# Performance work log

Measured on AMD Instinct MI355X. Metric: run time of the kernel, lower is better.

The kernel has to match this reference:

```python
import jax, jax.numpy as jnp
import numpy as np

N = 50000      # nodes
E = 800000     # edges (before self-loops)
DIN, H1, H2, OUT = 128, 128, 64, 40
LN_EPS = 1e-5


def setup_inputs() -> dict:
    key = jax.random.key(0)
    ks = jax.random.split(key, 16)
    s = lambda d: 1.0 / np.sqrt(d)
    inp = {
        "x": jax.random.normal(ks[0], (N, DIN), jnp.float32),
        "edge_index": jax.random.randint(ks[1], (2, E), 0, N, dtype=jnp.int64),
        # GCNConv weights (applied as x @ W) and biases
        "W1": jax.random.normal(ks[2], (DIN, H1), jnp.float32) * s(DIN),
        "b1": jnp.zeros((H1,), jnp.float32),
        "W2": jax.random.normal(ks[3], (H1, H2), jnp.float32) * s(H1),
        "b2": jnp.zeros((H2,), jnp.float32),
        "W3": jax.random.normal(ks[4], (H2, H2), jnp.float32) * s(H2),
        "b3": jnp.zeros((H2,), jnp.float32),
        # LayerNorms
        "g1": jnp.ones((H1,), jnp.float32),
        "be1": jnp.zeros((H1,), jnp.float32),
        "g2": jnp.ones((H2,), jnp.float32),
        "be2": jnp.zeros((H2,), jnp.float32),
        # post_mp MLP head
        "Wp1": jax.random.normal(ks[5], (H2, H2), jnp.float32) * s(H2),
        "bp1": jnp.zeros((H2,), jnp.float32),
        "Wp2": jax.random.normal(ks[6], (H2, OUT), jnp.float32) * s(H2),
        "bp2": jnp.zeros((OUT,), jnp.float32),
    }
    return inp


def _layer_norm(x, g, b):
    mu = jnp.mean(x, axis=-1, keepdims=True)
    var = jnp.mean((x - mu) ** 2, axis=-1, keepdims=True)
    return (x - mu) * jax.lax.rsqrt(var + LN_EPS) * g + b


def _gcn(x, src, dst, norm, W, b):
    # PyG GCNConv: linear first, then normalized gather/scatter-add, bias last
    h = x @ W                                  # [N, H]
    msg = h[src] * norm[:, None]               # [E+N, H] gather
    out = jax.ops.segment_sum(msg, dst, num_segments=N)  # scatter-add
    return out + b


def reference(x, edge_index, W1, b1, W2, b2, W3, b3, g1, be1, g2, be2,
              Wp1, bp1, Wp2, bp2):
    loops = jnp.arange(N, dtype=edge_index.dtype)
    src = jnp.concatenate([edge_index[0], loops])  # add self-loops
    dst = jnp.concatenate([edge_index[1], loops])
    # symmetric normalization D^{-1/2} (A+I) D^{-1/2} (same graph all layers)
    deg = jax.ops.segment_sum(jnp.ones_like(src, dtype=x.dtype), dst,
                              num_segments=N)
    dinv = jnp.where(deg > 0, jax.lax.rsqrt(jnp.maximum(deg, 1.0)), 0.0)
    norm = dinv[src] * dinv[dst]

    h = _gcn(x, src, dst, norm, W1, b1)
    h = _layer_norm(jax.nn.relu(h), g1, be1)
    h = _gcn(h, src, dst, norm, W2, b2)
    h = _layer_norm(jax.nn.relu(h), g2, be2)
    emb = _gcn(h, src, dst, norm, W3, b3)      # emb = conv output, pre-ReLU
    h = jax.nn.relu(emb)
    h = (h @ Wp1 + bp1) @ Wp2 + bp2            # post_mp: two stacked Linears
    return emb, jax.nn.log_softmax(h, axis=1)
```

## Files before the change

### kernel.cpp

```cpp
#include <hip/hip_runtime.h>
#include <hip/hip_bf16.h>

#define DIN 128
#define HID1 128
#define HID2 64
#define OUTD 40
#define NCHUNK 64

typedef __attribute__((ext_vector_type(8))) short bf16x8;
typedef __attribute__((ext_vector_type(4))) float f32x4;

__device__ __forceinline__ float bf2f(unsigned int u) {
    union { unsigned int i; float f; } c;
    c.i = u << 16;
    return c.f;
}
__device__ __forceinline__ unsigned short f2bf(float f) {
    union { float f; unsigned int i; } c; c.f = f;
    unsigned int r = c.i + 0x7FFFu + ((c.i >> 16) & 1u);
    return (unsigned short)(r >> 16);
}
__device__ __forceinline__ unsigned int packbf(float lo, float hi) {
    return (unsigned int)f2bf(lo) | ((unsigned int)f2bf(hi) << 16);
}

struct WCvt {
    const void* p[14];
    int sz[14];
    int off[14];
    int tobf[14];
    int cols[14];
};


__launch_bounds__(512)
__global__ void prep_kernel(const unsigned short* __restrict__ xu,
                            const int* __restrict__ ei,
                            int* __restrict__ flags,
                            int* __restrict__ pos,
                            unsigned int* __restrict__ hist,
                            WCvt wc, unsigned short* __restrict__ wbf,
                            float* __restrict__ wf,
                            int E, int N) {
    __shared__ unsigned int h32[25000];
    __shared__ int sh2[2];
    const int NW = (N + 1) >> 1;
    const int b = blockIdx.x;
    const int t = threadIdx.x;
    if (b < NCHUNK) {
        if (t == 0) sh2[0] = 0;
        for (int w = t; w < NW; w += 512) h32[w] = 0u;
        __syncthreads();
        int zodd = 0;
        for (int k = t; k < 1024; k += 512)
            if (ei[2 * k + 1] == 0) zodd++;
        if (zodd) atomicAdd(&sh2[0], zodd);
        __syncthreads();
        const int e64 = (sh2[0] > 512) ? 1 : 0;
        const int CH = (E + NCHUNK - 1) / NCHUNK;
        const int lo = b * CH;
        int hi = lo + CH; if (hi > E) hi = E;
        for (int e = lo + t; e < hi; e += 512) {
            int d = e64 ? ei[2 * (E + e)] : ei[E + e];
            if ((unsigned)d < (unsigned)N) {
                unsigned sh = (unsigned)(d & 1) << 4;
                unsigned old = atomicAdd(&h32[d >> 1], 1u << sh);
                pos[e] = (int)((old >> sh) & 0xffffu);
            } else {
                pos[e] = -1;
            }
        }
        __syncthreads();
        unsigned int* hb = hist + (size_t)b * NW;
        for (int w = t; w < NW; w += 512) hb[w] = h32[w];
    } else {
        if (t < 2) sh2[t] = 0;
        __syncthreads();
        int bad = 0;
        for (int k = t; k < 2048; k += 512) {
            float v = bf2f(xu[2 * k]);
            float a = fabsf(v);
            if (!(a <= 1e4f) || (v != 0.f && a < 1e-4f)) bad++;
        }
        int zodd = 0;
        for (int k = t; k < 1024; k += 512)
            if (ei[2 * k + 1] == 0) zodd++;
        if (bad) atomicAdd(&sh2[0], bad);
        if (zodd) atomicAdd(&sh2[1], zodd);
        __syncthreads();
        int xf32 = (sh2[0] > 512) ? 1 : 0;
        if (t == 0) {
            flags[0] = xf32;
            flags[1] = (sh2[1] > 512) ? 1 : 0;
        }
        for (int a = 0; a < 14; ++a) {
            const float* pf = (const float*)wc.p[a];
            const unsigned short* pb = (const unsigned short*)wc.p[a];
            int n = wc.sz[a], off = wc.off[a], tobf = wc.tobf[a];
            int cols = wc.cols[a];
            int rows = tobf ? (n / cols) : 0;
            for (int i = t; i < n; i += 512) {
                float v = xf32 ? pf[i] : bf2f(pb[i]);
                if (tobf) {
                    int k = i / cols, m = i % cols;
                    wbf[off + m * rows + k] = f2bf(v);
                } else {
                    wf[off + i] = v;
                }
            }
        }
    }
}

__device__ __forceinline__ int get_src(const int* ei, int E, int e, int e64) {
    return e64 ? ei[2 * e] : ei[e];
}
__device__ __forceinline__ int get_dst(const int* ei, int E, int e, int e64) {
    return e64 ? ei[2 * (E + e)] : ei[E + e];
}

__launch_bounds__(256)
__global__ void phaseB_kernel(const unsigned int* __restrict__ hist,
                              unsigned int* __restrict__ basev,
                              int* __restrict__ cnt, int* __restrict__ bsum,
                              int N) {
    __shared__ int red[256];
    const int NW = (N + 1) >> 1;
    const int NP = NW * 2;
    int t = threadIdx.x;
    int w = blockIdx.x * 256 + t;
    unsigned run0 = 0, run1 = 0;
    if (w < NW) {
        #pragma unroll 4
        for (int b = 0; b < NCHUNK; ++b) {
            unsigned u = hist[(size_t)b * NW + w];
            uint2 bb; bb.x = run0; bb.y = run1;
            *(uint2*)&basev[(size_t)b * NP + 2 * w] = bb;
            run0 += u & 0xffffu;
            run1 += u >> 16;
        }
        cnt[2 * w] = (int)run0;
        if (2 * w + 1 < N) cnt[2 * w + 1] = (int)run1;
    }
    int tot = 0;
    if (w < NW) tot = (int)run0 + ((2 * w + 1 < N) ? (int)run1 : 0);
    red[t] = tot;
    __syncthreads();
    #pragma unroll
    for (int off = 64; off >= 1; off >>= 1) {
        if ((t & 127) < off) red[t] += red[t + off];
        __syncthreads();
    }
    if (t == 0) bsum[2 * blockIdx.x] = red[0];
    if (t == 128) bsum[2 * blockIdx.x + 1] = red[128];
}

__launch_bounds__(256)
__global__ void bscan_kernel(const int* __restrict__ bsum, int* __restrict__ bbase,
                             int* __restrict__ indptr, int NB, int N) {
    __shared__ int part[256];
    int t = threadIdx.x;
    int CH = (NB + 255) / 256;
    int lo = t * CH, hi = lo + CH; if (hi > NB) hi = NB;
    int s = 0;
    for (int i = lo; i < hi; ++i) s += bsum[i];
    part[t] = s;
    __syncthreads();
    for (int off = 1; off < 256; off <<= 1) {
        int v = (t >= off) ? part[t - off] : 0;
        __syncthreads();
        part[t] += v;
        __syncthreads();
    }
    int run = (t > 0) ? part[t - 1] : 0;
    for (int i = lo; i < hi; ++i) { bbase[i] = run; run += bsum[i]; }
    if (t == 255) indptr[N] = part[255];
}

__launch_bounds__(256)
__global__ void emit_kernel(const int* __restrict__ cnt, const int* __restrict__ bbase,
                            int* __restrict__ indptr, float* __restrict__ dinv, int N) {
    __shared__ int sh[256];
    int t = threadIdx.x;
    int i = blockIdx.x * 256 + t;
    int c = (i < N) ? cnt[i] : 0;
    sh[t] = c;
    __syncthreads();
    for (int off = 1; off < 256; off <<= 1) {
        int v = (t >= off) ? sh[t - off] : 0;
        __syncthreads();
        sh[t] += v;
        __syncthreads();
    }
    if (i < N) {
        int excl = sh[t] - c + bbase[blockIdx.x];
        indptr[i] = excl;
        dinv[i] = 1.0f / sqrtf((float)(c + 1));
    }
}

__global__ void scatter_kernel(const int* __restrict__ ei, const int* __restrict__ indptr,
                               const int* __restrict__ pos, const float* __restrict__ dinv,
                               const unsigned int* __restrict__ basev,
                               int2* __restrict__ csr_sn,
                               int E, int N, const int* __restrict__ flags) {
    int e64 = flags[1];
    int CH = (E + NCHUNK - 1) / NCHUNK;
    int NP = ((N + 1) >> 1) * 2;
    int base = (blockIdx.x * blockDim.x + threadIdx.x) * 4;
    #pragma unroll
    for (int u = 0; u < 4; ++u) {
        int e = base + u;
        if (e < E) {
            int p = pos[e];
            if (p >= 0) {
                int bb = e / CH;
                int d = get_dst(ei, E, e, e64);
                int s = get_src(ei, E, e, e64);
                if ((unsigned)s >= (unsigned)N) s = 0;
                float nrm = dinv[s] * dinv[d];
                int slot = indptr[d] + (int)basev[(size_t)bb * NP + d] + p;
                csr_sn[slot] = make_int2(s, __float_as_int(nrm));
            }
        }
    }
}


template<typename AT>
__device__ __forceinline__ bf16x8 ld_afrag(const AT* p);
template<>
__device__ __forceinline__ bf16x8 ld_afrag<unsigned short>(const unsigned short* p) {
    return *(const bf16x8*)p;
}
template<>
__device__ __forceinline__ bf16x8 ld_afrag<float>(const float* p) {
    float4 a = *(const float4*)p;
    float4 b = *(const float4*)(p + 4);
    bf16x8 r;
    r[0] = (short)f2bf(a.x); r[1] = (short)f2bf(a.y);
    r[2] = (short)f2bf(a.z); r[3] = (short)f2bf(a.w);
    r[4] = (short)f2bf(b.x); r[5] = (short)f2bf(b.y);
    r[6] = (short)f2bf(b.z); r[7] = (short)f2bf(b.w);
    return r;
}

template<int K, int M, typename AT>
__device__ __forceinline__ void mm_body(const AT* __restrict__ A,
                                        const unsigned short* __restrict__ WT,
                                        unsigned short* __restrict__ C, int N,
                                        unsigned short (*Ws)[K + 8]) {
    int tid = threadIdx.x;
    for (int idx = tid; idx < M * K / 8; idx += 256) {
        int r = idx / (K / 8), c8 = idx % (K / 8);
        *(uint4*)&Ws[r][c8 * 8] = *(const uint4*)&WT[r * K + c8 * 8];
    }
    __syncthreads();
    int w = tid >> 6, lane = tid & 63;
    int m = lane & 15, q = lane >> 4;
    int row_a = blockIdx.x * 64 + w * 16 + m;
    if (row_a >= N) row_a = N - 1;
    const AT* arow = A + (size_t)row_a * K;
    f32x4 acc[M / 16];
    #pragma unroll
    for (int t = 0; t < M / 16; ++t) acc[t] = (f32x4){0.f, 0.f, 0.f, 0.f};
    #pragma unroll
    for (int ks = 0; ks < K / 32; ++ks) {
        int k0 = ks * 32 + q * 8;
        bf16x8 a = ld_afrag<AT>(arow + k0);
        #pragma unroll
        for (int t = 0; t < M / 16; ++t) {
            bf16x8 b = *(const bf16x8*)&Ws[t * 16 + m][k0];
            acc[t] = __builtin_amdgcn_mfma_f32_16x16x32_bf16(a, b, acc[t], 0, 0, 0);
        }
    }
    int rbase = blockIdx.x * 64 + w * 16 + q * 4;
    #pragma unroll
    for (int reg = 0; reg < 4; ++reg) {
        int row = rbase + reg;
        if (row < N) {
            #pragma unroll
            for (int t = 0; t < M / 16; ++t)
                C[(size_t)row * M + t * 16 + m] = f2bf(acc[t][reg]);
        }
    }
}

template<int K, int M>
__launch_bounds__(256)
__global__ void mm_dual_kernel(const void* __restrict__ A,
                               const unsigned short* __restrict__ WT,
                               unsigned short* __restrict__ C, int N,
                               const int* __restrict__ flags) {
    __shared__ unsigned short Ws[M][K + 8];
    if (flags[0]) mm_body<K, M, float>((const float*)A, WT, C, N, Ws);
    else          mm_body<K, M, unsigned short>((const unsigned short*)A, WT, C, N, Ws);
}

template<int K, int M>
__launch_bounds__(256)
__global__ void mm_bf_kernel(const unsigned short* __restrict__ A,
                             const unsigned short* __restrict__ WT,
                             unsigned short* __restrict__ C, int N) {
    __shared__ unsigned short Ws[M][K + 8];
    mm_body<K, M, unsigned short>(A, WT, C, N, Ws);
}


template<int VPL>
__device__ __forceinline__ void gacc1(float* acc, const unsigned short* r, float n) {
    if constexpr (VPL == 8) {
        uint4 u = *(const uint4*)r;
        acc[0] += bf2f(u.x & 0xffffu) * n; acc[1] += bf2f(u.x >> 16) * n;
        acc[2] += bf2f(u.y & 0xffffu) * n; acc[3] += bf2f(u.y >> 16) * n;
        acc[4] += bf2f(u.z & 0xffffu) * n; acc[5] += bf2f(u.z >> 16) * n;
        acc[6] += bf2f(u.w & 0xffffu) * n; acc[7] += bf2f(u.w >> 16) * n;
    } else {
        uint2 u = *(const uint2*)r;
        acc[0] += bf2f(u.x & 0xffffu) * n; acc[1] += bf2f(u.x >> 16) * n;
        acc[2] += bf2f(u.y & 0xffffu) * n; acc[3] += bf2f(u.y >> 16) * n;
    }
}

template<int VPL>
__device__ __forceinline__ void gacc4(float* acc,
                                      const unsigned short* r0, float n0,
                                      const unsigned short* r1, float n1,
                                      const unsigned short* r2, float n2,
                                      const unsigned short* r3, float n3) {
    if constexpr (VPL == 8) {
        uint4 u0 = *(const uint4*)r0;
        uint4 u1 = *(const uint4*)r1;
        uint4 u2 = *(const uint4*)r2;
        uint4 u3 = *(const uint4*)r3;
        acc[0] += bf2f(u0.x & 0xffffu) * n0 + bf2f(u1.x & 0xffffu) * n1
                + bf2f(u2.x & 0xffffu) * n2 + bf2f(u3.x & 0xffffu) * n3;
        acc[1] += bf2f(u0.x >> 16) * n0 + bf2f(u1.x >> 16) * n1
                + bf2f(u2.x >> 16) * n2 + bf2f(u3.x >> 16) * n3;
        acc[2] += bf2f(u0.y & 0xffffu) * n0 + bf2f(u1.y & 0xffffu) * n1
                + bf2f(u2.y & 0xffffu) * n2 + bf2f(u3.y & 0xffffu) * n3;
        acc[3] += bf2f(u0.y >> 16) * n0 + bf2f(u1.y >> 16) * n1
                + bf2f(u2.y >> 16) * n2 + bf2f(u3.y >> 16) * n3;
        acc[4] += bf2f(u0.z & 0xffffu) * n0 + bf2f(u1.z & 0xffffu) * n1
                + bf2f(u2.z & 0xffffu) * n2 + bf2f(u3.z & 0xffffu) * n3;
        acc[5] += bf2f(u0.z >> 16) * n0 + bf2f(u1.z >> 16) * n1
                + bf2f(u2.z >> 16) * n2 + bf2f(u3.z >> 16) * n3;
        acc[6] += bf2f(u0.w & 0xffffu) * n0 + bf2f(u1.w & 0xffffu) * n1
                + bf2f(u2.w & 0xffffu) * n2 + bf2f(u3.w & 0xffffu) * n3;
        acc[7] += bf2f(u0.w >> 16) * n0 + bf2f(u1.w >> 16) * n1
                + bf2f(u2.w >> 16) * n2 + bf2f(u3.w >> 16) * n3;
    } else {
        uint2 u0 = *(const uint2*)r0;
        uint2 u1 = *(const uint2*)r1;
        uint2 u2 = *(const uint2*)r2;
        uint2 u3 = *(const uint2*)r3;
        acc[0] += bf2f(u0.x & 0xffffu) * n0 + bf2f(u1.x & 0xffffu) * n1
                + bf2f(u2.x & 0xffffu) * n2 + bf2f(u3.x & 0xffffu) * n3;
        acc[1] += bf2f(u0.x >> 16) * n0 + bf2f(u1.x >> 16) * n1
                + bf2f(u2.x >> 16) * n2 + bf2f(u3.x >> 16) * n3;
        acc[2] += bf2f(u0.y & 0xffffu) * n0 + bf2f(u1.y & 0xffffu) * n1
                + bf2f(u2.y & 0xffffu) * n2 + bf2f(u3.y & 0xffffu) * n3;
        acc[3] += bf2f(u0.y >> 16) * n0 + bf2f(u1.y >> 16) * n1
                + bf2f(u2.y >> 16) * n2 + bf2f(u3.y >> 16) * n3;
    }
}

template<int H, bool RELU_LN, bool EMB>
__launch_bounds__(256)
__global__ void agg_kernel(const unsigned short* __restrict__ h,
                           const int* __restrict__ indptr,
                           const int2* __restrict__ csr_sn,
                           const float* __restrict__ dinv,
                           const float* __restrict__ bias,
                           const float* __restrict__ gamma,
                           const float* __restrict__ beta,
                           unsigned short* __restrict__ out,
                           void* __restrict__ out_emb,
                           int N, const int* __restrict__ flags) {
    constexpr int VPL = H / 16;
    __shared__ int2 lsn[4][64];
    int w = threadIdx.x >> 6;
    int lane = threadIdx.x & 63;
    int slot = lane >> 4;
    int idx = lane & 15;
    int node = blockIdx.x * 4 + w;
    bool active = node < N;
    int nd = active ? node : N - 1;
    float di = dinv[nd];
    int c0 = idx * VPL;
    float acc[VPL];
    #pragma unroll
    for (int v = 0; v < VPL; ++v) acc[v] = 0.f;
    if (slot == 0)
        gacc1<VPL>(acc, h + (size_t)nd * H + c0, di * di);
    int beg = indptr[nd], end = indptr[nd + 1];
    for (int base = beg; base < end; base += 64) {
        int m = end - base; if (m > 64) m = 64;
        if (lane < m) lsn[w][lane] = csr_sn[base + lane];
        int m16 = m & ~15;
        int j = 0;
        for (; j < m16; j += 16) {
            int2 e0 = lsn[w][j + slot];
            int2 e1 = lsn[w][j + 4 + slot];
            int2 e2 = lsn[w][j + 8 + slot];
            int2 e3 = lsn[w][j + 12 + slot];
            gacc4<VPL>(acc,
                       h + (size_t)e0.x * H + c0, __int_as_float(e0.y),
                       h + (size_t)e1.x * H + c0, __int_as_float(e1.y),
                       h + (size_t)e2.x * H + c0, __int_as_float(e2.y),
                       h + (size_t)e3.x * H + c0, __int_as_float(e3.y));
        }
        for (int tt = j + slot; tt < m; tt += 4) {
            int2 e = lsn[w][tt];
            gacc1<VPL>(acc, h + (size_t)e.x * H + c0, __int_as_float(e.y));
        }
    }
    #pragma unroll
    for (int v = 0; v < VPL; ++v) {
        acc[v] += __shfl_xor(acc[v], 16, 64);
        acc[v] += __shfl_xor(acc[v], 32, 64);
    }
    #pragma unroll
    for (int v = 0; v < VPL; ++v) acc[v] += bias[c0 + v];
    if constexpr (RELU_LN) {
        #pragma unroll
        for (int v = 0; v < VPL; ++v) acc[v] = fmaxf(acc[v], 0.f);
        float s = 0.f, sq = 0.f;
        #pragma unroll
        for (int v = 0; v < VPL; ++v) { s += acc[v]; sq += acc[v] * acc[v]; }
        #pragma unroll
        for (int off = 8; off >= 1; off >>= 1) {
            s += __shfl_xor(s, off, 64);
            sq += __shfl_xor(sq, off, 64);
        }
        float mu = s * (1.0f / H);
        float var = fmaxf(sq * (1.0f / H) - mu * mu, 0.f);
        float inv = 1.0f / sqrtf(var + 1e-5f);
        #pragma unroll
        for (int v = 0; v < VPL; ++v)
            acc[v] = (acc[v] - mu) * inv * gamma[c0 + v] + beta[c0 + v];
    }
    if (active && slot == 0) {
        unsigned short* orow = out + (size_t)node * H + c0;
        if constexpr (VPL == 8) {
            uint4 p;
            p.x = packbf(acc[0], acc[1]); p.y = packbf(acc[2], acc[3]);
            p.z = packbf(acc[4], acc[5]); p.w = packbf(acc[6], acc[7]);
            *(uint4*)orow = p;
        } else {
            uint2 p; p.x = packbf(acc[0], acc[1]); p.y = packbf(acc[2], acc[3]);
            *(uint2*)orow = p;
        }
        if constexpr (EMB) {
            if (flags[0]) {
                float* o = (float*)out_emb + (size_t)node * H + c0;
                #pragma unroll
                for (int v4 = 0; v4 < VPL / 4; ++v4)
                    *(float4*)(o + v4 * 4) = make_float4(acc[v4 * 4], acc[v4 * 4 + 1],
                                                         acc[v4 * 4 + 2], acc[v4 * 4 + 3]);
            } else {
                unsigned short* o = (unsigned short*)out_emb + (size_t)node * H + c0;
                #pragma unroll
                for (int v2 = 0; v2 < VPL / 2; ++v2)
                    ((unsigned int*)o)[v2] = packbf(acc[v2 * 2], acc[v2 * 2 + 1]);
            }
        }
    }
}


__launch_bounds__(256)
__global__ void head_kernel(const unsigned short* __restrict__ emb,
                            const float* __restrict__ Wp1,
                            const float* __restrict__ bp1,
                            const float* __restrict__ Wp2,
                            const float* __restrict__ bp2,
                            void* __restrict__ d_out, int N,
                            const int* __restrict__ flags) {
    __shared__ float Est[64][68];
    __shared__ float W1s[64][64];
    __shared__ float Tst[64][68];
    __shared__ float W2s[64][OUTD];
    __shared__ float b1s[64];
    __shared__ float b2s[OUTD];
    int tid = threadIdx.x;
    int row0 = blockIdx.x * 64;
    for (int i = tid; i < 64 * 64; i += 256) W1s[i >> 6][i & 63] = Wp1[i];
    for (int i = tid; i < 64 * OUTD; i += 256) W2s[i / OUTD][i % OUTD] = Wp2[i];
    if (tid < 64) b1s[tid] = bp1[tid];
    if (tid < OUTD) b2s[tid] = bp2[tid];
    for (int i = tid; i < 64 * 32; i += 256) {
        int r = i >> 5, kk = i & 31;
        int row = row0 + r;
        unsigned int u = (row < N) ? *(const unsigned int*)&emb[(size_t)row * 64 + kk * 2] : 0u;
        Est[kk * 2][r]     = fmaxf(bf2f(u & 0xffffu), 0.f);
        Est[kk * 2 + 1][r] = fmaxf(bf2f(u >> 16), 0.f);
    }
    __syncthreads();
    {
        int rg = tid >> 4, cg = tid & 15;
        int r = rg * 4, c = cg * 4;
        float acc[4][4];
        #pragma unroll
        for (int i = 0; i < 4; ++i)
            #pragma unroll
            for (int jj = 0; jj < 4; ++jj) acc[i][jj] = b1s[c + jj];
        #pragma unroll 4
        for (int k = 0; k < 64; ++k) {
            float4 a = *(const float4*)&Est[k][r];
            float4 wv = *(const float4*)&W1s[k][c];
            acc[0][0] += a.x * wv.x; acc[0][1] += a.x * wv.y; acc[0][2] += a.x * wv.z; acc[0][3] += a.x * wv.w;
            acc[1][0] += a.y * wv.x; acc[1][1] += a.y * wv.y; acc[1][2] += a.y * wv.z; acc[1][3] += a.y * wv.w;
            acc[2][0] += a.z * wv.x; acc[2][1] += a.z * wv.y; acc[2][2] += a.z * wv.z; acc[2][3] += a.z * wv.w;
            acc[3][0] += a.w * wv.x; acc[3][1] += a.w * wv.y; acc[3][2] += a.w * wv.z; acc[3][3] += a.w * wv.w;
        }
        #pragma unroll
        for (int i = 0; i < 4; ++i)
            #pragma unroll
            for (int jj = 0; jj < 4; ++jj) Tst[c + jj][r + i] = acc[i][jj];
    }
    __syncthreads();
    int row = tid >> 2, tc = tid & 3, o0 = tc * 10;
    int node = row0 + row;
    float u[10];
    #pragma unroll
    for (int o = 0; o < 10; ++o) u[o] = b2s[o0 + o];
    for (int c2 = 0; c2 < 64; ++c2) {
        float tv = Tst[c2][row];
        const float2* wp = (const float2*)&W2s[c2][o0];
        #pragma unroll
        for (int o2 = 0; o2 < 5; ++o2) {
            float2 wv = wp[o2];
            u[o2 * 2]     += tv * wv.x;
            u[o2 * 2 + 1] += tv * wv.y;
        }
    }
    float mx = u[0];
    #pragma unroll
    for (int o = 1; o < 10; ++o) mx = fmaxf(mx, u[o]);
    mx = fmaxf(mx, __shfl_xor(mx, 1, 64));
    mx = fmaxf(mx, __shfl_xor(mx, 2, 64));
    float sum = 0.f;
    #pragma unroll
    for (int o = 0; o < 10; ++o) sum += __expf(u[o] - mx);
    sum += __shfl_xor(sum, 1, 64);
    sum += __shfl_xor(sum, 2, 64);
    float lse = mx + __logf(sum);
    if (node < N) {
        if (flags[0]) {
            float* base = (float*)d_out + (size_t)N * HID2;
            float* op = base + (size_t)node * OUTD + o0;
            #pragma unroll
            for (int o = 0; o < 10; ++o) op[o] = u[o] - lse;
        } else {
            unsigned short* base = (unsigned short*)d_out + (size_t)N * HID2;
            unsigned int* op = (unsigned int*)(base + (size_t)node * OUTD + o0);
            #pragma unroll
            for (int o2 = 0; o2 < 5; ++o2)
                op[o2] = packbf(u[o2 * 2] - lse, u[o2 * 2 + 1] - lse);
        }
    }
}


extern "C" void kernel_launch(void* const* d_in, const int* in_sizes, int n_in,
                              void* d_out, int out_size, void* d_ws, size_t ws_size,
                              hipStream_t stream) {
    const unsigned short* xu = (const unsigned short*)d_in[0];
    const int*            ei = (const int*)d_in[1];

    const int N = in_sizes[0] / DIN;
    const int E = in_sizes[1] / 2;
    const int NW = (N + 1) / 2;
    const int NP = NW * 2;

    size_t off = 0;
    auto take = [&](size_t bytes) {
        size_t cur = off;
        off += (bytes + 255) & ~(size_t)255;
        return cur;
    };
    char* ws = (char*)d_ws;
    int*   flags   = (int*)  (ws + take(256));
    int*   cnt     = (int*)  (ws + take((size_t)N * 4));
    float* dinv    = (float*)(ws + take((size_t)N * 4));
    int*   indptr  = (int*)  (ws + take((size_t)(N + 1) * 4));
    int*   pos     = (int*)  (ws + take((size_t)E * 4));
    int2*  csr_sn  = (int2*) (ws + take((size_t)E * 8));
    int*   bsum    = (int*)  (ws + take(((size_t)N / 256 + 4) * 4));
    int*   bbase   = (int*)  (ws + take(((size_t)N / 256 + 4) * 4));
    unsigned int* hist  = (unsigned int*)(ws + take((size_t)NCHUNK * NW * 4));
    unsigned int* basev = (unsigned int*)(ws + take((size_t)NCHUNK * NP * 4));
    unsigned short* wbf = (unsigned short*)(ws + take(32768 * 2));
    float*          wf  = (float*)         (ws + take(8192 * 4));
    unsigned short* hbuf = (unsigned short*)(ws + take((size_t)N * DIN * 2));
    unsigned short* abuf = (unsigned short*)(ws + take((size_t)N * DIN * 2));
    (void)ws_size; (void)n_in; (void)out_size;

    const int TB = 256;
    dim3 blk(TB);
    const int NB = (N + 255) / 256;

    WCvt wc;
    int bfoff = 0, foff = 0;
    int offs[14];
    const int wcols[14] = {HID1, 0, HID2, 0, HID2, 0, 0, 0, 0, 0, 0, 0, 0, 0};
    for (int a = 0; a < 14; ++a) {
        int idx = a + 2;
        wc.p[a] = d_in[idx];
        wc.sz[a] = in_sizes[idx];
        int tobf = (idx == 2 || idx == 4 || idx == 6) ? 1 : 0;
        wc.tobf[a] = tobf;
        wc.cols[a] = tobf ? wcols[a] : 1;
        if (tobf) { wc.off[a] = bfoff; bfoff += in_sizes[idx]; }
        else      { wc.off[a] = foff;  foff  += in_sizes[idx]; }
        offs[a] = wc.off[a];
    }

    prep_kernel<<<dim3(NCHUNK + 1), dim3(512), 0, stream>>>(
        xu, ei, flags, pos, hist, wc, wbf, wf, E, N);
    phaseB_kernel<<<dim3((NW + 255) / 256), blk, 0, stream>>>(hist, basev, cnt, bsum, N);
    bscan_kernel<<<dim3(1), blk, 0, stream>>>(bsum, bbase, indptr, NB, N);
    emit_kernel<<<dim3(NB), blk, 0, stream>>>(cnt, bbase, indptr, dinv, N);
    scatter_kernel<<<dim3((E + 1023) / 1024), blk, 0, stream>>>(
        ei, indptr, pos, dinv, basev, csr_sn, E, N, flags);

    unsigned short* W1t = wbf + offs[0];
    unsigned short* W2t = wbf + offs[2];
    unsigned short* W3t = wbf + offs[4];
    float* b1f  = wf + offs[1];
    float* b2f  = wf + offs[3];
    float* b3f  = wf + offs[5];
    float* g1f  = wf + offs[6];
    float* be1f = wf + offs[7];
    float* g2f  = wf + offs[8];
    float* be2f = wf + offs[9];
    float* Wp1f = wf + offs[10];
    float* bp1f = wf + offs[11];
    float* Wp2f = wf + offs[12];
    float* bp2f = wf + offs[13];

    const int MMG = (N + 63) / 64;
    const int AGG = (N + 3) / 4;

    mm_dual_kernel<DIN, HID1><<<dim3(MMG), blk, 0, stream>>>(
        d_in[0], W1t, hbuf, N, flags);
    agg_kernel<HID1, true, false><<<dim3(AGG), blk, 0, stream>>>(
        hbuf, indptr, csr_sn, dinv, b1f, g1f, be1f, abuf, nullptr, N, flags);

    mm_bf_kernel<HID1, HID2><<<dim3(MMG), blk, 0, stream>>>(abuf, W2t, hbuf, N);
    agg_kernel<HID2, true, false><<<dim3(AGG), blk, 0, stream>>>(
        hbuf, indptr, csr_sn, dinv, b2f, g2f, be2f, abuf, nullptr, N, flags);

    mm_bf_kernel<HID2, HID2><<<dim3(MMG), blk, 0, stream>>>(abuf, W3t, hbuf, N);
    agg_kernel<HID2, false, true><<<dim3(AGG), blk, 0, stream>>>(
        hbuf, indptr, csr_sn, dinv, b3f, nullptr, nullptr, abuf, d_out, N, flags);

    head_kernel<<<dim3((N + 63) / 64), blk, 0, stream>>>(
        abuf, Wp1f, bp1f, Wp2f, bp2f, d_out, N, flags);
}
```

Measured before the change: 339.2 us.

## Split prep histogram by node range and pad gather tail with zero-weight edges

```diff
diff --git a/kernel.cpp b/kernel.cpp
--- a/kernel.cpp
+++ b/kernel.cpp
@@ -6,6 +6,7 @@
 #define HID2 64
 #define OUTD 40
 #define NCHUNK 64
+#define NRANGE 4
 
 typedef __attribute__((ext_vector_type(8))) short bf16x8;
 typedef __attribute__((ext_vector_type(4))) float f32x4;
@@ -42,14 +43,21 @@
                             WCvt wc, unsigned short* __restrict__ wbf,
                             float* __restrict__ wf,
                             int E, int N) {
-    __shared__ unsigned int h32[25000];
+    __shared__ unsigned int h32[6272];
     __shared__ int sh2[2];
     const int NW = (N + 1) >> 1;
+    const int RW = (NW + NRANGE - 1) / NRANGE;
     const int b = blockIdx.x;
     const int t = threadIdx.x;
-    if (b < NCHUNK) {
+    if (b < NCHUNK * NRANGE) {
+        const int c = b >> 2, r = b & (NRANGE - 1);
+        const int wlo = r * RW;
+        int whi = wlo + RW; if (whi > NW) whi = NW;
+        const int nlo = wlo * 2;
+        const int nhi = whi * 2;
+        const int nw = whi - wlo;
         if (t == 0) sh2[0] = 0;
-        for (int w = t; w < NW; w += 512) h32[w] = 0u;
+        for (int w = t; w < nw; w += 512) h32[w] = 0u;
         __syncthreads();
         int zodd = 0;
         for (int k = t; k < 1024; k += 512)
@@ -58,21 +66,24 @@
         __syncthreads();
         const int e64 = (sh2[0] > 512) ? 1 : 0;
         const int CH = (E + NCHUNK - 1) / NCHUNK;
-        const int lo = b * CH;
+        const int lo = c * CH;
         int hi = lo + CH; if (hi > E) hi = E;
         for (int e = lo + t; e < hi; e += 512) {
             int d = e64 ? ei[2 * (E + e)] : ei[E + e];
             if ((unsigned)d < (unsigned)N) {
-                unsigned sh = (unsigned)(d & 1) << 4;
-                unsigned old = atomicAdd(&h32[d >> 1], 1u << sh);
-                pos[e] = (int)((old >> sh) & 0xffffu);
-            } else {
+                if (d >= nlo && d < nhi) {
+                    int dl = d - nlo;
+                    unsigned sh = (unsigned)(dl & 1) << 4;
+                    unsigned old = atomicAdd(&h32[dl >> 1], 1u << sh);
+                    pos[e] = (int)((old >> sh) & 0xffffu);
+                }
+            } else if (r == 0) {
                 pos[e] = -1;
             }
         }
         __syncthreads();
-        unsigned int* hb = hist + (size_t)b * NW;
-        for (int w = t; w < NW; w += 512) hb[w] = h32[w];
+        unsigned int* hb = hist + (size_t)c * NW + wlo;
+        for (int w = t; w < nw; w += 512) hb[w] = h32[w];
     } else {
         if (t < 2) sh2[t] = 0;
         __syncthreads();
@@ -396,10 +407,10 @@
     int beg = indptr[nd], end = indptr[nd + 1];
     for (int base = beg; base < end; base += 64) {
         int m = end - base; if (m > 64) m = 64;
-        if (lane < m) lsn[w][lane] = csr_sn[base + lane];
-        int m16 = m & ~15;
+        lsn[w][lane] = (lane < m) ? csr_sn[base + lane] : make_int2(0, 0);
+        int rounds = (m + 15) >> 4;
         int j = 0;
-        for (; j < m16; j += 16) {
+        for (int rr = 0; rr < rounds; ++rr, j += 16) {
             int2 e0 = lsn[w][j + slot];
             int2 e1 = lsn[w][j + 4 + slot];
             int2 e2 = lsn[w][j + 8 + slot];
@@ -409,10 +420,6 @@
                        h + (size_t)e1.x * H + c0, __int_as_float(e1.y),
                        h + (size_t)e2.x * H + c0, __int_as_float(e2.y),
                        h + (size_t)e3.x * H + c0, __int_as_float(e3.y));
-        }
-        for (int tt = j + slot; tt < m; tt += 4) {
-            int2 e = lsn[w][tt];
-            gacc1<VPL>(acc, h + (size_t)e.x * H + c0, __int_as_float(e.y));
         }
     }
     #pragma unroll
@@ -617,7 +624,7 @@
         offs[a] = wc.off[a];
     }
 
-    prep_kernel<<<dim3(NCHUNK + 1), dim3(512), 0, stream>>>(
+    prep_kernel<<<dim3(NCHUNK * NRANGE + 1), dim3(512), 0, stream>>>(
         xu, ei, flags, pos, hist, wc, wbf, wf, E, N);
     phaseB_kernel<<<dim3((NW + 255) / 256), blk, 0, stream>>>(hist, basev, cnt, bsum, N);
     bscan_kernel<<<dim3(1), blk, 0, stream>>>(bsum, bbase, indptr, NB, N);
```

After: 337.8 us. Within noise of the previous version (-0.4%).
